# Optimization experiments

Hardware: AMD Instinct MI355X
Metric: run time of the kernel (lower is better)

The kernel has to match this reference:

```python
import jax, jax.numpy as jnp
import numpy as np

V, E, H, D = 32000, 512, 512, 3          # vocab, embed_dim, hidden_dim, max_depth
PD = max(H // 4, 16)                      # policy depth-embed dim = 128
DEPTH_EMBED_SCALE = 0.01
SIB_SCALE = 1.0 / np.sqrt(H)              # sibling_scale default 1/sqrt(hidden_dim)
GREEDY_THRESHOLD = 0.5
PROB_MIN, PROB_MAX = 1e-7, 1.0 - 1e-7


def _ln(x, g, b, eps=1e-5):
    m = x.mean(-1, keepdims=True)
    v = jnp.var(x, axis=-1, keepdims=True)
    return (x - m) * jax.lax.rsqrt(v + eps) * g + b


def setup_inputs() -> dict:
    key = jax.random.key(0)
    ks = jax.random.split(key, 12)
    def n(k, shape, s=0.02):
        return jax.random.normal(k, shape, jnp.float32) * s
    return {
        "token_ids": jax.random.randint(ks[0], (4096,), 0, V),
        "emb": n(ks[1], (V, E)),                      # embedding table
        "proj_w": n(ks[2], (H, E), 0.04), "proj_b": jnp.zeros(H, jnp.float32),
        "cf_w": n(ks[3], (2 * H, H), 0.04), "cf_b": jnp.zeros(2 * H, jnp.float32),
        "in_g": jnp.ones(H, jnp.float32), "in_b": jnp.zeros(H, jnp.float32),   # policy input LayerNorm
        "pde": n(ks[4], (D + 1, PD), 0.01),           # policy depth embedding
        "f1w": n(ks[5], (H // 2, H + PD), 0.04), "f1b": jnp.zeros(H // 2, jnp.float32),
        "n1g": jnp.ones(H // 2, jnp.float32), "n1b": jnp.zeros(H // 2, jnp.float32),
        "f2w": n(ks[6], (H // 4, H // 2), 0.06), "f2b": jnp.zeros(H // 4, jnp.float32),
        "n2g": jnp.ones(H // 4, jnp.float32), "n2b": jnp.zeros(H // 4, jnp.float32),
        "pow_w": n(ks[7], (1, H // 4), 0.01), "pow_b": jnp.zeros(1, jnp.float32),
        "sib": n(ks[8], (2, H)),                      # sibling embeddings (left/right)
        "dep": n(ks[9], (D + 1, H), 0.01),            # tree depth embeddings
        "out_w": n(ks[10], (V, H), 0.04), "out_b": jnp.zeros(V, jnp.float32),
    }


def _forward(token_ids, emb, proj_w, proj_b, cf_w, cf_b, in_g, in_b, pde,
             f1w, f1b, n1g, n1b, f2w, f2b, n2g, n2b, pow_w, pow_b,
             sib, dep, out_w, out_b):
    # h0: project token embeddings to hidden space. [N, H]
    h0 = emb[token_ids] @ proj_w.T + proj_b
    nodes = h0[None]                      # level-0 nodes: [1, N, H]
    agg_sum = h0                          # running sum over all tree nodes
    agg_cnt = jnp.float32(1.0)
    alive = jnp.float32(1.0)              # cumulative greedy-expand mask
    for level in range(D):
        # growth policy on the level-mean hidden (+ scaled depth embedding)
        lh = nodes.mean(0) + DEPTH_EMBED_SCALE * dep[level]          # [N, H]
        hn = _ln(lh, in_g, in_b)
        de = jnp.broadcast_to(pde[min(level, D)], (hn.shape[0], PD))
        x = jnp.concatenate([hn, de], axis=-1)
        x = jax.nn.relu(_ln(x @ f1w.T + f1b, n1g, n1b))
        x = jax.nn.relu(_ln(x @ f2w.T + f2b, n2g, n2b))
        p = jax.nn.sigmoid((x @ pow_w.T + pow_b)[..., 0])             # [N]
        p_mean = jnp.clip(p, PROB_MIN, PROB_MAX).mean()
        alive = alive * (p_mean >= GREEDY_THRESHOLD).astype(jnp.float32)
        # binary child expansion: child_fc then chunk into left/right + sibling embeds
        cf = jnp.einsum('mnh,kh->mnk', nodes, cf_w) + cf_b            # [M, N, 2H]
        left = cf[..., :H] + SIB_SCALE * sib[0]
        right = cf[..., H:] + SIB_SCALE * sib[1]
        nodes = jnp.concatenate([left, right], axis=0)                # [2M, N, H]
        agg_sum = agg_sum + alive * nodes.sum(0)
        agg_cnt = agg_cnt + alive * jnp.float32(nodes.shape[0])
    pooled = agg_sum / jnp.maximum(agg_cnt, 1e-8)                     # mean pooling
    return pooled @ out_w.T + out_b                                   # [N, V]


def reference(token_ids, emb, proj_w, proj_b, cf_w, cf_b, in_g, in_b, pde,
              f1w, f1b, n1g, n1b, f2w, f2b, n2g, n2b, pow_w, pow_b,
              sib, dep, out_w, out_b):
    return _forward(token_ids, emb, proj_w, proj_b, cf_w, cf_b, in_g, in_b, pde,
                    f1w, f1b, n1g, n1b, f2w, f2b, n2g, n2b, pow_w, pow_b,
                    sib, dep, out_w, out_b)
```

## Files before the change

### kernel.cpp

```cpp
#include <hip/hip_runtime.h>

typedef unsigned short u16;
using bf16x8 = __attribute__((ext_vector_type(8))) short;
using f32x4  = __attribute__((ext_vector_type(4))) float;

#define SIB_SCALE_F 0.04419417382415922f

__device__ __forceinline__ u16 f2b(float f) {
  unsigned u = __builtin_bit_cast(unsigned, f);
  return (u16)((u + 0x7FFFu + ((u >> 16) & 1u)) >> 16);
}

__device__ __forceinline__ float wred(float v) {
  #pragma unroll
  for (int m = 1; m < 64; m <<= 1) v += __shfl_xor(v, m);
  return v;
}

__device__ __forceinline__ void gload16(const void* g, void* l) {
  __builtin_amdgcn_global_load_lds(
      (const __attribute__((address_space(1))) unsigned int*)g,
      (__attribute__((address_space(3))) unsigned int*)l, 16, 0, 0);
}

__global__ __launch_bounds__(512, 2) void gemmP(
    const u16* __restrict__ A, const u16* __restrict__ B,
    const float* __restrict__ bias,
    float* __restrict__ C, int M, int N, int K, int MT)
{
  __shared__ u16 lds[65536];
  const int t = threadIdx.x, w = t >> 6, lane = t & 63;
  const int wm = w >> 2, wn = w & 3;
  const int r16 = lane & 15, ks = lane >> 4;

  const int bn = blockIdx.y * 256;
  const int mg = blockIdx.x;
  const int NT = K >> 6;

  auto stageH = [&](const u16* __restrict__ G, int grow0, int kt, int half, int opBase) {
    const int k0 = kt << 6;
    u16* dst = lds + opBase + ((kt & 1) << 14) + (half << 13);
    #pragma unroll
    for (int j = 0; j < 2; ++j) {
      const int r = half * 128 + j * 64 + w * 8 + (lane >> 3);
      const int s = (lane & 7) ^ (r & 7);
      gload16(G + (size_t)(grow0 + r) * K + k0 + s * 8,
              dst + j * 4096 + w * 512);
    }
  };

  for (int mt = 0; mt < MT; ++mt) {
    const int bm = (mg * MT + mt) * 256;

    f32x4 acc[8][4];
    #pragma unroll
    for (int m = 0; m < 8; ++m)
      #pragma unroll
      for (int n = 0; n < 4; ++n) {
        f32x4 z = {0.f, 0.f, 0.f, 0.f};
        acc[m][n] = z;
      }

    __builtin_amdgcn_sched_barrier(0);
    stageH(A, bm, 0, 0, 0);
    stageH(A, bm, 0, 1, 0);
    stageH(B, bn, 0, 0, 32768);
    stageH(B, bn, 0, 1, 32768);
    __builtin_amdgcn_sched_barrier(0);
    stageH(B, bn, 1, 0, 32768);
    stageH(B, bn, 1, 1, 32768);
    asm volatile("s_waitcnt vmcnt(4)" ::: "memory");
    __builtin_amdgcn_sched_barrier(0);
    __builtin_amdgcn_s_barrier();

    for (int kt = 0; kt < NT; ++kt) {
      const u16* Ab = lds + ((kt & 1) << 14);
      const u16* Bb = lds + 32768 + ((kt & 1) << 14);
      bf16x8 bfr[4][2];

      #pragma unroll
      for (int p = 0; p < 4; ++p) {
        bf16x8 af2[2][2];
        #pragma unroll
        for (int i = 0; i < 2; ++i) {
          const int row = wm * 128 + (2 * p + i) * 16 + r16;
          af2[i][0] = *(const bf16x8*)(Ab + row * 64 + ((ks ^ (row & 7)) << 3));
          af2[i][1] = *(const bf16x8*)(Ab + row * 64 + (((4 + ks) ^ (row & 7)) << 3));
        }
        if (p == 0) {
          #pragma unroll
          for (int n = 0; n < 4; ++n) {
            const int row = wn * 64 + n * 16 + r16;
            bfr[n][0] = *(const bf16x8*)(Bb + row * 64 + ((ks ^ (row & 7)) << 3));
            bfr[n][1] = *(const bf16x8*)(Bb + row * 64 + (((4 + ks) ^ (row & 7)) << 3));
          }
        }
        if (p == 0 && kt + 1 < NT) stageH(A, bm, kt + 1, 0, 0);
        if (p == 1 && kt + 1 < NT) stageH(A, bm, kt + 1, 1, 0);
        if (p == 2 && kt + 2 < NT) stageH(B, bn, kt + 2, 0, 32768);
        if (p == 3) {
          if (kt + 2 < NT) {
            stageH(B, bn, kt + 2, 1, 32768);
            asm volatile("s_waitcnt vmcnt(4)" ::: "memory");
          } else {
            asm volatile("s_waitcnt vmcnt(0)" ::: "memory");
          }
          __builtin_amdgcn_sched_barrier(0);
        }
        __builtin_amdgcn_s_barrier();
        asm volatile("s_waitcnt lgkmcnt(0)" ::: "memory");
        __builtin_amdgcn_sched_barrier(0);
        __builtin_amdgcn_s_setprio(1);
        #pragma unroll
        for (int i = 0; i < 2; ++i)
          #pragma unroll
          for (int n = 0; n < 4; ++n) {
            acc[2 * p + i][n] = __builtin_amdgcn_mfma_f32_16x16x32_bf16(
                bfr[n][0], af2[i][0], acc[2 * p + i][n], 0, 0, 0);
            acc[2 * p + i][n] = __builtin_amdgcn_mfma_f32_16x16x32_bf16(
                bfr[n][1], af2[i][1], acc[2 * p + i][n], 0, 0, 0);
          }
        __builtin_amdgcn_s_setprio(0);
        __builtin_amdgcn_s_barrier();
      }
    }

    #pragma unroll
    for (int m = 0; m < 8; ++m) {
      const int grow = bm + wm * 128 + m * 16 + r16;
      float* Crow = C + (size_t)grow * N;
      #pragma unroll
      for (int n = 0; n < 4; ++n) {
        const int gcol = bn + wn * 64 + n * 16 + ks * 4;
        const float4 bv = *(const float4*)(bias + gcol);
        float4 o;
        o.x = acc[m][n][0] + bv.x;
        o.y = acc[m][n][1] + bv.y;
        o.z = acc[m][n][2] + bv.z;
        o.w = acc[m][n][3] + bv.w;
        *(float4*)(Crow + gcol) = o;
      }
    }
  }
}

template <bool GATHER>
__global__ __launch_bounds__(256) void gemm_bf16_bt(
    const float* __restrict__ Afp, const int* __restrict__ tok,
    const u16* __restrict__ A, const u16* __restrict__ B,
    const float* __restrict__ bias, int blvl, float bscale,
    float* __restrict__ C, u16* __restrict__ Cb,
    int M, int N, int K)
{
  __shared__ u16 ldsA[128 * 32];
  __shared__ u16 ldsB[128 * 32];
  const int t = threadIdx.x;
  const int w = t >> 6;
  const int lane = t & 63;
  const int wr = w >> 1, wc = w & 1;

  const int nb = gridDim.x * gridDim.y;
  const int lid = blockIdx.y * gridDim.x + blockIdx.x;
  const int chunk = nb >> 3;
  const int nlid = (lid & 7) * chunk + (lid >> 3);
  const int bx = nlid % gridDim.x, by = nlid / gridDim.x;

  const int bm = bx * 128, bn = by * 128;
  const int r16 = lane & 15, ks = lane >> 4;
  const int srow = t >> 2, sslot = t & 3;

  f32x4 acc[4][4];
  #pragma unroll
  for (int m = 0; m < 4; ++m)
    #pragma unroll
    for (int n = 0; n < 4; ++n) {
      f32x4 z = {0.f, 0.f, 0.f, 0.f};
      acc[m][n] = z;
    }

  for (int k0 = 0; k0 < K; k0 += 32) {
    if (k0) __syncthreads();
    #pragma unroll
    for (int i = 0; i < 2; ++i) {
      const int row = srow + i * 64;
      const int sl = sslot ^ ((row >> 1) & 3);
      if constexpr (GATHER) {
        const float* src = Afp + (size_t)tok[bm + row] * 512 + k0 + sl * 8;
        const float4 a0 = *(const float4*)src;
        const float4 a1 = *(const float4*)(src + 4);
        bf16x8 v;
        v[0] = (short)f2b(a0.x); v[1] = (short)f2b(a0.y);
        v[2] = (short)f2b(a0.z); v[3] = (short)f2b(a0.w);
        v[4] = (short)f2b(a1.x); v[5] = (short)f2b(a1.y);
        v[6] = (short)f2b(a1.z); v[7] = (short)f2b(a1.w);
        *(bf16x8*)(ldsA + i * 2048 + w * 512 + lane * 8) = v;
      } else {
        gload16(A + (size_t)(bm + row) * K + k0 + sl * 8,
                ldsA + (i * 2048 + w * 512));
      }
      gload16(B + (size_t)(bn + row) * K + k0 + sl * 8,
              ldsB + (i * 2048 + w * 512));
    }
    __syncthreads();

    bf16x8 af[4], bfr[4];
    #pragma unroll
    for (int m = 0; m < 4; ++m) {
      const int row = wr * 64 + m * 16 + r16;
      af[m] = *(const bf16x8*)(ldsA + row * 32 + ((ks ^ ((row >> 1) & 3)) << 3));
    }
    #pragma unroll
    for (int n = 0; n < 4; ++n) {
      const int row = wc * 64 + n * 16 + r16;
      bfr[n] = *(const bf16x8*)(ldsB + row * 32 + ((ks ^ ((row >> 1) & 3)) << 3));
    }
    #pragma unroll
    for (int m = 0; m < 4; ++m)
      #pragma unroll
      for (int n = 0; n < 4; ++n)
        acc[m][n] = __builtin_amdgcn_mfma_f32_16x16x32_bf16(bfr[n], af[m], acc[m][n], 0, 0, 0);
  }

  const float* be = bias + (size_t)(bm >> 12) * blvl;
  #pragma unroll
  for (int m = 0; m < 4; ++m) {
    const int grow = bm + wr * 64 + m * 16 + r16;
    #pragma unroll
    for (int n = 0; n < 4; ++n) {
      const int gcol = bn + wc * 64 + n * 16 + ks * 4;
      const float4 bv = *(const float4*)(be + gcol);
      float4 o;
      o.x = acc[m][n][0] + bv.x * bscale;
      o.y = acc[m][n][1] + bv.y * bscale;
      o.z = acc[m][n][2] + bv.z * bscale;
      o.w = acc[m][n][3] + bv.w * bscale;
      const size_t idx = (size_t)grow * N + gcol;
      *(float4*)(C + idx) = o;
      if (Cb) {
        ushort4 ob = { f2b(o.x), f2b(o.y), f2b(o.z), f2b(o.w) };
        *(ushort4*)(Cb + idx) = ob;
      }
    }
  }
}

__global__ __launch_bounds__(256) void prep_misc(
    const float* __restrict__ cf_w, const float* __restrict__ cf_b,
    const float* __restrict__ sib, const float* __restrict__ proj_w,
    const float* __restrict__ f1w, const float* __restrict__ f1b,
    const float* __restrict__ f2w, const float* __restrict__ pde,
    u16* __restrict__ wsum_b, u16* __restrict__ projw_b,
    u16* __restrict__ f1w512b, u16* __restrict__ f2wb,
    float* __restrict__ cvec, float* __restrict__ psum,
    float* __restrict__ y1bias)
{
  const int b = blockIdx.x, t = threadIdx.x;
  if (b < 256) {
    const int idx = b * 256 + t;
    const float4 a = ((const float4*)cf_w)[idx];
    const float4 c = ((const float4*)(cf_w + 262144))[idx];
    ushort4 o = { f2b(a.x + c.x), f2b(a.y + c.y), f2b(a.z + c.z), f2b(a.w + c.w) };
    ((ushort4*)wsum_b)[idx] = o;
  } else if (b < 512) {
    const int idx = (b - 256) * 256 + t;
    const float4 v = ((const float4*)proj_w)[idx];
    ushort4 o = { f2b(v.x), f2b(v.y), f2b(v.z), f2b(v.w) };
    ((ushort4*)projw_b)[idx] = o;
  } else if (b < 640) {
    const int fi = (b - 512) * 256 + t;
    const int row = fi >> 7, c4 = fi & 127;
    const float4 v = *(const float4*)(f1w + (size_t)row * 640 + c4 * 4);
    ushort4 o = { f2b(v.x), f2b(v.y), f2b(v.z), f2b(v.w) };
    ((ushort4*)f1w512b)[row * 128 + c4] = o;
  } else if (b < 672) {
    const int idx = (b - 640) * 256 + t;
    const float4 v = ((const float4*)f2w)[idx];
    ushort4 o = { f2b(v.x), f2b(v.y), f2b(v.z), f2b(v.w) };
    ((ushort4*)f2wb)[idx] = o;
  } else if (b < 675) {
    const int l = b - 672, j = t;
    const float* wrow = f1w + (size_t)j * 640 + 512;
    const float* p = pde + l * 128;
    float s = f1b[j];
    #pragma unroll 4
    for (int k = 0; k < 128; ++k) s += wrow[k] * p[k];
    y1bias[l * 256 + j] = s;
  } else {
    cvec[t]       = cf_b[t]       + cf_b[512 + t] + SIB_SCALE_F * (sib[t]       + sib[512 + t]);
    cvec[256 + t] = cf_b[256 + t] + cf_b[768 + t] + SIB_SCALE_F * (sib[256 + t] + sib[768 + t]);
    if (t < 3) psum[t] = 0.f;
  }
}

__global__ __launch_bounds__(256) void mean_ln_concat_b(
    const float* __restrict__ S0, const float* __restrict__ S1,
    const float* __restrict__ S2,
    const float* __restrict__ dep,
    const float* __restrict__ g, const float* __restrict__ b,
    u16* __restrict__ X)
{
  const int wid = threadIdx.x >> 6, lane = threadIdx.x & 63;
  const int gr = blockIdx.x * 4 + wid;
  const int l = gr >> 12, n = gr & 4095;
  const float* Sr = (l == 0 ? S0 : l == 1 ? S1 : S2) + (size_t)n * 512;
  const float invM = (l == 0 ? 1.f : l == 1 ? 0.5f : 0.25f);
  const float* depl = dep + 512 * l;
  const int c0 = lane * 8;
  float x[8];
  float s = 0.f, sq = 0.f;
  #pragma unroll
  for (int i = 0; i < 8; ++i) {
    const float v = Sr[c0 + i] * invM + 0.01f * depl[c0 + i];
    x[i] = v; s += v; sq += v * v;
  }
  s = wred(s); sq = wred(sq);
  const float mean = s * (1.f / 512.f);
  const float var = sq * (1.f / 512.f) - mean * mean;
  const float rs = rsqrtf(var + 1e-5f);
  ushort4 o0, o1;
  o0.x = f2b((x[0] - mean) * rs * g[c0 + 0] + b[c0 + 0]);
  o0.y = f2b((x[1] - mean) * rs * g[c0 + 1] + b[c0 + 1]);
  o0.z = f2b((x[2] - mean) * rs * g[c0 + 2] + b[c0 + 2]);
  o0.w = f2b((x[3] - mean) * rs * g[c0 + 3] + b[c0 + 3]);
  o1.x = f2b((x[4] - mean) * rs * g[c0 + 4] + b[c0 + 4]);
  o1.y = f2b((x[5] - mean) * rs * g[c0 + 5] + b[c0 + 5]);
  o1.z = f2b((x[6] - mean) * rs * g[c0 + 6] + b[c0 + 6]);
  o1.w = f2b((x[7] - mean) * rs * g[c0 + 7] + b[c0 + 7]);
  ushort4* Xr = (ushort4*)(X + (size_t)gr * 512);
  Xr[lane * 2]     = o0;
  Xr[lane * 2 + 1] = o1;
}

__global__ __launch_bounds__(256) void ln_relu_b256(
    const float* __restrict__ X, const float* __restrict__ g,
    const float* __restrict__ b, u16* __restrict__ O)
{
  const int wid = threadIdx.x >> 6, lane = threadIdx.x & 63;
  const int n = blockIdx.x * 4 + wid;
  const float* Xr = X + (size_t)n * 256;
  float x[4];
  float s = 0.f, sq = 0.f;
  #pragma unroll
  for (int i = 0; i < 4; ++i) {
    x[i] = Xr[lane * 4 + i]; s += x[i]; sq += x[i] * x[i];
  }
  s = wred(s); sq = wred(sq);
  const float mean = s * (1.f / 256.f);
  const float var = sq * (1.f / 256.f) - mean * mean;
  const float rs = rsqrtf(var + 1e-5f);
  ushort4 o;
  o.x = f2b(fmaxf((x[0] - mean) * rs * g[lane * 4 + 0] + b[lane * 4 + 0], 0.f));
  o.y = f2b(fmaxf((x[1] - mean) * rs * g[lane * 4 + 1] + b[lane * 4 + 1], 0.f));
  o.z = f2b(fmaxf((x[2] - mean) * rs * g[lane * 4 + 2] + b[lane * 4 + 2], 0.f));
  o.w = f2b(fmaxf((x[3] - mean) * rs * g[lane * 4 + 3] + b[lane * 4 + 3], 0.f));
  ((ushort4*)(O + (size_t)n * 256))[lane] = o;
}

__global__ __launch_bounds__(256) void ln_relu128(
    float* __restrict__ X, const float* __restrict__ g, const float* __restrict__ b)
{
  const int wid = threadIdx.x >> 6, lane = threadIdx.x & 63;
  const int n = blockIdx.x * 4 + wid;
  float* Xr = X + (size_t)n * 128;
  float x[2];
  float s = 0.f, sq = 0.f;
  #pragma unroll
  for (int i = 0; i < 2; ++i) {
    x[i] = Xr[lane * 2 + i]; s += x[i]; sq += x[i] * x[i];
  }
  s = wred(s); sq = wred(sq);
  const float mean = s * (1.f / 128.f);
  const float var = sq * (1.f / 128.f) - mean * mean;
  const float rs = rsqrtf(var + 1e-5f);
  #pragma unroll
  for (int i = 0; i < 2; ++i) {
    const int c = lane * 2 + i;
    Xr[c] = fmaxf((x[i] - mean) * rs * g[c] + b[c], 0.f);
  }
}

__global__ __launch_bounds__(256) void policy_reduce_b(
    const float* __restrict__ Y2, const float* __restrict__ pw,
    const float* __restrict__ pb, float* __restrict__ psum)
{
  __shared__ float part[4];
  const int wid = threadIdx.x >> 6, lane = threadIdx.x & 63;
  const int gr = blockIdx.x * 4 + wid;
  const float* r = Y2 + (size_t)gr * 128;
  float z = r[lane * 2] * pw[lane * 2] + r[lane * 2 + 1] * pw[lane * 2 + 1];
  z = wred(z);
  if (lane == 0) {
    const float p = 1.f / (1.f + expf(-(z + pb[0])));
    part[wid] = fminf(fmaxf(p, 1e-7f), 1.f - 1e-7f);
  }
  __syncthreads();
  if (threadIdx.x == 0)
    atomicAdd(psum + (gr >> 12), part[0] + part[1] + part[2] + part[3]);
}

__global__ void finalize_coef(const float* __restrict__ psum, float* __restrict__ coef)
{
  float alive = 1.f, cnt = 1.f;
  #pragma unroll
  for (int l = 0; l < 3; ++l) {
    const float pm = psum[l] * (1.f / 4096.f);
    if (!(pm >= 0.5f)) alive = 0.f;
    coef[l] = alive;
    cnt += alive * (float)(2 << l);
  }
  coef[3] = 1.f / fmaxf(cnt, 1e-8f);
}

__global__ __launch_bounds__(256) void pool_to_bf16(
    const float* __restrict__ h0, const float* __restrict__ S1,
    const float* __restrict__ S2, const float* __restrict__ S3,
    const float* __restrict__ coef, u16* __restrict__ P)
{
  const int idx = blockIdx.x * 256 + threadIdx.x;
  const float c0 = coef[0], c1 = coef[1], c2 = coef[2], inv = coef[3];
  const float4 a  = ((const float4*)h0)[idx];
  const float4 s1 = ((const float4*)S1)[idx];
  const float4 s2 = ((const float4*)S2)[idx];
  const float4 s3 = ((const float4*)S3)[idx];
  ushort4 o;
  o.x = f2b((a.x + c0 * s1.x + c1 * s2.x + c2 * s3.x) * inv);
  o.y = f2b((a.y + c0 * s1.y + c1 * s2.y + c2 * s3.y) * inv);
  o.z = f2b((a.z + c0 * s1.z + c1 * s2.z + c2 * s3.z) * inv);
  o.w = f2b((a.w + c0 * s1.w + c1 * s2.w + c2 * s3.w) * inv);
  ((ushort4*)P)[idx] = o;
}

__global__ __launch_bounds__(256) void f32_to_bf16_vec(
    const float* __restrict__ src, u16* __restrict__ dst, int n4)
{
  const int idx = blockIdx.x * 256 + threadIdx.x;
  if (idx >= n4) return;
  const float4 v = ((const float4*)src)[idx];
  ushort4 o = { f2b(v.x), f2b(v.y), f2b(v.z), f2b(v.w) };
  ((ushort4*)dst)[idx] = o;
}

extern "C" void kernel_launch(void* const* d_in, const int* in_sizes, int n_in,
                              void* d_out, int out_size, void* d_ws, size_t ws_size,
                              hipStream_t stream) {
  const int*   tok    = (const int*)  d_in[0];
  const float* emb    = (const float*)d_in[1];
  const float* proj_w = (const float*)d_in[2];
  const float* proj_b = (const float*)d_in[3];
  const float* cf_w   = (const float*)d_in[4];
  const float* cf_b   = (const float*)d_in[5];
  const float* in_g   = (const float*)d_in[6];
  const float* in_b   = (const float*)d_in[7];
  const float* pde    = (const float*)d_in[8];
  const float* f1w    = (const float*)d_in[9];
  const float* f1b    = (const float*)d_in[10];
  const float* n1g    = (const float*)d_in[11];
  const float* n1b    = (const float*)d_in[12];
  const float* f2w    = (const float*)d_in[13];
  const float* f2bias = (const float*)d_in[14];
  const float* n2g    = (const float*)d_in[15];
  const float* n2b    = (const float*)d_in[16];
  const float* pow_w  = (const float*)d_in[17];
  const float* pow_b  = (const float*)d_in[18];
  const float* sib    = (const float*)d_in[19];
  const float* dep    = (const float*)d_in[20];
  const float* out_w  = (const float*)d_in[21];
  const float* out_b  = (const float*)d_in[22];
  float* out = (float*)d_out;

  char* ws = (char*)d_ws;
  size_t off = 0;
  auto alloc = [&](size_t bytes) -> void* {
    void* p = ws + off;
    off += (bytes + 255) & ~(size_t)255;
    return p;
  };
  u16*   outw_b  = (u16*)  alloc((size_t)32000 * 512 * 2);
  u16*   projw_b = (u16*)  alloc((size_t)512 * 512 * 2);
  u16*   wsum_b  = (u16*)  alloc((size_t)512 * 512 * 2);
  u16*   f1w512b = (u16*)  alloc((size_t)256 * 512 * 2);
  u16*   f2wb    = (u16*)  alloc((size_t)128 * 256 * 2);
  float* h0f     = (float*)alloc((size_t)4096 * 512 * 4);
  u16*   h0b     = (u16*)  alloc((size_t)4096 * 512 * 2);
  float* S1f     = (float*)alloc((size_t)4096 * 512 * 4);
  u16*   S1b     = (u16*)  alloc((size_t)4096 * 512 * 2);
  float* S2f     = (float*)alloc((size_t)4096 * 512 * 4);
  u16*   S2b     = (u16*)  alloc((size_t)4096 * 512 * 2);
  float* S3f     = (float*)alloc((size_t)4096 * 512 * 4);
  u16*   S3b     = (u16*)  alloc((size_t)4096 * 512 * 2);
  u16*   X       = (u16*)  alloc((size_t)12288 * 512 * 2);
  float* Y1      = (float*)alloc((size_t)12288 * 256 * 4);
  u16*   Y1b     = (u16*)  alloc((size_t)12288 * 256 * 2);
  float* Y2      = (float*)alloc((size_t)12288 * 128 * 4);
  float* y1bias  = (float*)alloc(3 * 256 * 4);
  float* cvec    = (float*)alloc(512 * 4);
  float* psum    = (float*)alloc(256);
  float* coef    = (float*)alloc(256);
  u16*   poolb   = (u16*)  alloc((size_t)4096 * 512 * 2);

  prep_misc<<<676, 256, 0, stream>>>(cf_w, cf_b, sib, proj_w, f1w, f1b, f2w, pde,
                                     wsum_b, projw_b, f1w512b, f2wb,
                                     cvec, psum, y1bias);
  f32_to_bf16_vec<<<16000, 256, 0, stream>>>(out_w, outw_b, 4096000);

  gemm_bf16_bt<true><<<dim3(32, 4), 256, 0, stream>>>(
      emb, tok, nullptr, projw_b, proj_b, 0, 1.f, h0f, h0b, 4096, 512, 512);
  gemm_bf16_bt<false><<<dim3(32, 4), 256, 0, stream>>>(
      nullptr, nullptr, h0b, wsum_b, cvec, 0, 1.f, S1f, S1b, 4096, 512, 512);
  gemm_bf16_bt<false><<<dim3(32, 4), 256, 0, stream>>>(
      nullptr, nullptr, S1b, wsum_b, cvec, 0, 2.f, S2f, S2b, 4096, 512, 512);
  gemm_bf16_bt<false><<<dim3(32, 4), 256, 0, stream>>>(
      nullptr, nullptr, S2b, wsum_b, cvec, 0, 4.f, S3f, S3b, 4096, 512, 512);

  mean_ln_concat_b<<<3072, 256, 0, stream>>>(h0f, S1f, S2f, dep, in_g, in_b, X);
  gemm_bf16_bt<false><<<dim3(96, 2), 256, 0, stream>>>(
      nullptr, nullptr, X, f1w512b, y1bias, 256, 1.f, Y1, nullptr, 12288, 256, 512);
  ln_relu_b256<<<3072, 256, 0, stream>>>(Y1, n1g, n1b, Y1b);
  gemm_bf16_bt<false><<<dim3(96, 1), 256, 0, stream>>>(
      nullptr, nullptr, Y1b, f2wb, f2bias, 0, 1.f, Y2, nullptr, 12288, 128, 256);
  ln_relu128<<<3072, 256, 0, stream>>>(Y2, n2g, n2b);
  policy_reduce_b<<<3072, 256, 0, stream>>>(Y2, pow_w, pow_b, psum);
  finalize_coef<<<1, 1, 0, stream>>>(psum, coef);

  pool_to_bf16<<<2048, 256, 0, stream>>>(h0f, S1f, S2f, S3f, coef, poolb);

  gemmP<<<dim3(2, 125), 512, 0, stream>>>(poolb, outw_b, out_b,
                                          out, 4096, 32000, 512, 8);
}
```

Measured before the change: 424.4 us.

## Fuse pooling into level-3 GEMM epilogue and merge policy LN, reduce, and conversion kernels

Moves the level-3 child GEMM after the policy network and gives it an epilogue that computes the alive flags from psum and writes the pooled bf16 output directly. This removes the S3 fp32/bf16 buffers and the separate finalize_coef and pool_to_bf16 kernels. It also fuses ln_relu128 with policy_reduce into one kernel, avoiding the Y2 write-back and re-read. The out_w bf16 conversion is folded into prep_misc as extra blocks. Together these cut kernel launches and memory traffic, at the cost of a heavier GEMM epilogue that reads three fp32 tensors.

```diff
diff --git a/kernel.cpp b/kernel.cpp
--- a/kernel.cpp
+++ b/kernel.cpp
@@ -144,12 +144,15 @@
   }
 }
 
-template <bool GATHER>
+template <bool GATHER, bool POOL>
 __global__ __launch_bounds__(256) void gemm_bf16_bt(
     const float* __restrict__ Afp, const int* __restrict__ tok,
     const u16* __restrict__ A, const u16* __restrict__ B,
     const float* __restrict__ bias, int blvl, float bscale,
     float* __restrict__ C, u16* __restrict__ Cb,
+    const float* __restrict__ h0f, const float* __restrict__ S1f,
+    const float* __restrict__ S2f, const float* __restrict__ psum,
+    u16* __restrict__ P,
     int M, int N, int K)
 {
   __shared__ u16 ldsA[128 * 32];
@@ -222,6 +225,16 @@
   }
 
   const float* be = bias + (size_t)(bm >> 12) * blvl;
+
+  float a0 = 0.f, a1 = 0.f, a2 = 0.f, inv = 0.f;
+  if constexpr (POOL) {
+    a0 = (psum[0] * (1.f / 4096.f) >= 0.5f) ? 1.f : 0.f;
+    a1 = a0 * ((psum[1] * (1.f / 4096.f) >= 0.5f) ? 1.f : 0.f);
+    a2 = a1 * ((psum[2] * (1.f / 4096.f) >= 0.5f) ? 1.f : 0.f);
+    const float cnt = 1.f + a0 * 2.f + a1 * 4.f + a2 * 8.f;
+    inv = 1.f / fmaxf(cnt, 1e-8f);
+  }
+
   #pragma unroll
   for (int m = 0; m < 4; ++m) {
     const int grow = bm + wr * 64 + m * 16 + r16;
@@ -235,10 +248,22 @@
       o.z = acc[m][n][2] + bv.z * bscale;
       o.w = acc[m][n][3] + bv.w * bscale;
       const size_t idx = (size_t)grow * N + gcol;
-      *(float4*)(C + idx) = o;
-      if (Cb) {
-        ushort4 ob = { f2b(o.x), f2b(o.y), f2b(o.z), f2b(o.w) };
-        *(ushort4*)(Cb + idx) = ob;
+      if constexpr (POOL) {
+        const float4 h = *(const float4*)(h0f + idx);
+        const float4 s1 = *(const float4*)(S1f + idx);
+        const float4 s2 = *(const float4*)(S2f + idx);
+        ushort4 ob;
+        ob.x = f2b((h.x + a0 * s1.x + a1 * s2.x + a2 * o.x) * inv);
+        ob.y = f2b((h.y + a0 * s1.y + a1 * s2.y + a2 * o.y) * inv);
+        ob.z = f2b((h.z + a0 * s1.z + a1 * s2.z + a2 * o.z) * inv);
+        ob.w = f2b((h.w + a0 * s1.w + a1 * s2.w + a2 * o.w) * inv);
+        *(ushort4*)(P + idx) = ob;
+      } else {
+        *(float4*)(C + idx) = o;
+        if (Cb) {
+          ushort4 ob = { f2b(o.x), f2b(o.y), f2b(o.z), f2b(o.w) };
+          *(ushort4*)(Cb + idx) = ob;
+        }
       }
     }
   }
@@ -249,13 +274,19 @@
     const float* __restrict__ sib, const float* __restrict__ proj_w,
     const float* __restrict__ f1w, const float* __restrict__ f1b,
     const float* __restrict__ f2w, const float* __restrict__ pde,
+    const float* __restrict__ out_w,
     u16* __restrict__ wsum_b, u16* __restrict__ projw_b,
     u16* __restrict__ f1w512b, u16* __restrict__ f2wb,
     float* __restrict__ cvec, float* __restrict__ psum,
-    float* __restrict__ y1bias)
+    float* __restrict__ y1bias, u16* __restrict__ outw_b)
 {
   const int b = blockIdx.x, t = threadIdx.x;
-  if (b < 256) {
+  if (b >= 676) {
+    const int idx = (b - 676) * 256 + t;
+    const float4 v = ((const float4*)out_w)[idx];
+    ushort4 o = { f2b(v.x), f2b(v.y), f2b(v.z), f2b(v.w) };
+    ((ushort4*)outw_b)[idx] = o;
+  } else if (b < 256) {
     const int idx = b * 256 + t;
     const float4 a = ((const float4*)cf_w)[idx];
     const float4 c = ((const float4*)(cf_w + 262144))[idx];
@@ -356,38 +387,32 @@
   ((ushort4*)(O + (size_t)n * 256))[lane] = o;
 }
 
-__global__ __launch_bounds__(256) void ln_relu128(
-    float* __restrict__ X, const float* __restrict__ g, const float* __restrict__ b)
-{
-  const int wid = threadIdx.x >> 6, lane = threadIdx.x & 63;
-  const int n = blockIdx.x * 4 + wid;
-  float* Xr = X + (size_t)n * 128;
-  float x[2];
-  float s = 0.f, sq = 0.f;
-  #pragma unroll
-  for (int i = 0; i < 2; ++i) {
-    x[i] = Xr[lane * 2 + i]; s += x[i]; sq += x[i] * x[i];
-  }
-  s = wred(s); sq = wred(sq);
-  const float mean = s * (1.f / 128.f);
-  const float var = sq * (1.f / 128.f) - mean * mean;
-  const float rs = rsqrtf(var + 1e-5f);
-  #pragma unroll
-  for (int i = 0; i < 2; ++i) {
-    const int c = lane * 2 + i;
-    Xr[c] = fmaxf((x[i] - mean) * rs * g[c] + b[c], 0.f);
-  }
-}
-
-__global__ __launch_bounds__(256) void policy_reduce_b(
-    const float* __restrict__ Y2, const float* __restrict__ pw,
+__global__ __launch_bounds__(256) void ln_policy128(
+    const float* __restrict__ Y2, const float* __restrict__ g,
+    const float* __restrict__ b, const float* __restrict__ pw,
     const float* __restrict__ pb, float* __restrict__ psum)
 {
   __shared__ float part[4];
   const int wid = threadIdx.x >> 6, lane = threadIdx.x & 63;
   const int gr = blockIdx.x * 4 + wid;
-  const float* r = Y2 + (size_t)gr * 128;
-  float z = r[lane * 2] * pw[lane * 2] + r[lane * 2 + 1] * pw[lane * 2 + 1];
+  const float* Xr = Y2 + (size_t)gr * 128;
+  float x[2];
+  float s = 0.f, sq = 0.f;
+  #pragma unroll
+  for (int i = 0; i < 2; ++i) {
+    x[i] = Xr[lane * 2 + i]; s += x[i]; sq += x[i] * x[i];
+  }
+  s = wred(s); sq = wred(sq);
+  const float mean = s * (1.f / 128.f);
+  const float var = sq * (1.f / 128.f) - mean * mean;
+  const float rs = rsqrtf(var + 1e-5f);
+  float z = 0.f;
+  #pragma unroll
+  for (int i = 0; i < 2; ++i) {
+    const int c = lane * 2 + i;
+    const float v = fmaxf((x[i] - mean) * rs * g[c] + b[c], 0.f);
+    z += v * pw[c];
+  }
   z = wred(z);
   if (lane == 0) {
     const float p = 1.f / (1.f + expf(-(z + pb[0])));
@@ -396,48 +421,6 @@
   __syncthreads();
   if (threadIdx.x == 0)
     atomicAdd(psum + (gr >> 12), part[0] + part[1] + part[2] + part[3]);
-}
-
-__global__ void finalize_coef(const float* __restrict__ psum, float* __restrict__ coef)
-{
-  float alive = 1.f, cnt = 1.f;
-  #pragma unroll
-  for (int l = 0; l < 3; ++l) {
-    const float pm = psum[l] * (1.f / 4096.f);
-    if (!(pm >= 0.5f)) alive = 0.f;
-    coef[l] = alive;
-    cnt += alive * (float)(2 << l);
-  }
-  coef[3] = 1.f / fmaxf(cnt, 1e-8f);
-}
-
-__global__ __launch_bounds__(256) void pool_to_bf16(
-    const float* __restrict__ h0, const float* __restrict__ S1,
-    const float* __restrict__ S2, const float* __restrict__ S3,
-    const float* __restrict__ coef, u16* __restrict__ P)
-{
-  const int idx = blockIdx.x * 256 + threadIdx.x;
-  const float c0 = coef[0], c1 = coef[1], c2 = coef[2], inv = coef[3];
-  const float4 a  = ((const float4*)h0)[idx];
-  const float4 s1 = ((const float4*)S1)[idx];
-  const float4 s2 = ((const float4*)S2)[idx];
-  const float4 s3 = ((const float4*)S3)[idx];
-  ushort4 o;
-  o.x = f2b((a.x + c0 * s1.x + c1 * s2.x + c2 * s3.x) * inv);
-  o.y = f2b((a.y + c0 * s1.y + c1 * s2.y + c2 * s3.y) * inv);
-  o.z = f2b((a.z + c0 * s1.z + c1 * s2.z + c2 * s3.z) * inv);
-  o.w = f2b((a.w + c0 * s1.w + c1 * s2.w + c2 * s3.w) * inv);
-  ((ushort4*)P)[idx] = o;
-}
-
-__global__ __launch_bounds__(256) void f32_to_bf16_vec(
-    const float* __restrict__ src, u16* __restrict__ dst, int n4)
-{
-  const int idx = blockIdx.x * 256 + threadIdx.x;
-  if (idx >= n4) return;
-  const float4 v = ((const float4*)src)[idx];
-  ushort4 o = { f2b(v.x), f2b(v.y), f2b(v.z), f2b(v.w) };
-  ((ushort4*)dst)[idx] = o;
 }
 
 extern "C" void kernel_launch(void* const* d_in, const int* in_sizes, int n_in,
@@ -486,8 +469,6 @@
   u16*   S1b     = (u16*)  alloc((size_t)4096 * 512 * 2);
   float* S2f     = (float*)alloc((size_t)4096 * 512 * 4);
   u16*   S2b     = (u16*)  alloc((size_t)4096 * 512 * 2);
-  float* S3f     = (float*)alloc((size_t)4096 * 512 * 4);
-  u16*   S3b     = (u16*)  alloc((size_t)4096 * 512 * 2);
   u16*   X       = (u16*)  alloc((size_t)12288 * 512 * 2);
   float* Y1      = (float*)alloc((size_t)12288 * 256 * 4);
   u16*   Y1b     = (u16*)  alloc((size_t)12288 * 256 * 2);
@@ -495,34 +476,36 @@
   float* y1bias  = (float*)alloc(3 * 256 * 4);
   float* cvec    = (float*)alloc(512 * 4);
   float* psum    = (float*)alloc(256);
-  float* coef    = (float*)alloc(256);
   u16*   poolb   = (u16*)  alloc((size_t)4096 * 512 * 2);
 
-  prep_misc<<<676, 256, 0, stream>>>(cf_w, cf_b, sib, proj_w, f1w, f1b, f2w, pde,
-                                     wsum_b, projw_b, f1w512b, f2wb,
-                                     cvec, psum, y1bias);
-  f32_to_bf16_vec<<<16000, 256, 0, stream>>>(out_w, outw_b, 4096000);
-
-  gemm_bf16_bt<true><<<dim3(32, 4), 256, 0, stream>>>(
-      emb, tok, nullptr, projw_b, proj_b, 0, 1.f, h0f, h0b, 4096, 512, 512);
-  gemm_bf16_bt<false><<<dim3(32, 4), 256, 0, stream>>>(
-      nullptr, nullptr, h0b, wsum_b, cvec, 0, 1.f, S1f, S1b, 4096, 512, 512);
-  gemm_bf16_bt<false><<<dim3(32, 4), 256, 0, stream>>>(
-      nullptr, nullptr, S1b, wsum_b, cvec, 0, 2.f, S2f, S2b, 4096, 512, 512);
-  gemm_bf16_bt<false><<<dim3(32, 4), 256, 0, stream>>>(
-      nullptr, nullptr, S2b, wsum_b, cvec, 0, 4.f, S3f, S3b, 4096, 512, 512);
+  prep_misc<<<16676, 256, 0, stream>>>(cf_w, cf_b, sib, proj_w, f1w, f1b, f2w,
+                                       pde, out_w,
+                                       wsum_b, projw_b, f1w512b, f2wb,
+                                       cvec, psum, y1bias, outw_b);
+
+  gemm_bf16_bt<true, false><<<dim3(32, 4), 256, 0, stream>>>(
+      emb, tok, nullptr, projw_b, proj_b, 0, 1.f, h0f, h0b,
+      nullptr, nullptr, nullptr, nullptr, nullptr, 4096, 512, 512);
+  gemm_bf16_bt<false, false><<<dim3(32, 4), 256, 0, stream>>>(
+      nullptr, nullptr, h0b, wsum_b, cvec, 0, 1.f, S1f, S1b,
+      nullptr, nullptr, nullptr, nullptr, nullptr, 4096, 512, 512);
+  gemm_bf16_bt<false, false><<<dim3(32, 4), 256, 0, stream>>>(
+      nullptr, nullptr, S1b, wsum_b, cvec, 0, 2.f, S2f, S2b,
+      nullptr, nullptr, nullptr, nullptr, nullptr, 4096, 512, 512);
 
   mean_ln_concat_b<<<3072, 256, 0, stream>>>(h0f, S1f, S2f, dep, in_g, in_b, X);
-  gemm_bf16_bt<false><<<dim3(96, 2), 256, 0, stream>>>(
-      nullptr, nullptr, X, f1w512b, y1bias, 256, 1.f, Y1, nullptr, 12288, 256, 512);
+  gemm_bf16_bt<false, false><<<dim3(96, 2), 256, 0, stream>>>(
+      nullptr, nullptr, X, f1w512b, y1bias, 256, 1.f, Y1, nullptr,
+      nullptr, nullptr, nullptr, nullptr, nullptr, 12288, 256, 512);
   ln_relu_b256<<<3072, 256, 0, stream>>>(Y1, n1g, n1b, Y1b);
-  gemm_bf16_bt<false><<<dim3(96, 1), 256, 0, stream>>>(
-      nullptr, nullptr, Y1b, f2wb, f2bias, 0, 1.f, Y2, nullptr, 12288, 128, 256);
-  ln_relu128<<<3072, 256, 0, stream>>>(Y2, n2g, n2b);
-  policy_reduce_b<<<3072, 256, 0, stream>>>(Y2, pow_w, pow_b, psum);
-  finalize_coef<<<1, 1, 0, stream>>>(psum, coef);
-
-  pool_to_bf16<<<2048, 256, 0, stream>>>(h0f, S1f, S2f, S3f, coef, poolb);
+  gemm_bf16_bt<false, false><<<dim3(96, 1), 256, 0, stream>>>(
+      nullptr, nullptr, Y1b, f2wb, f2bias, 0, 1.f, Y2, nullptr,
+      nullptr, nullptr, nullptr, nullptr, nullptr, 12288, 128, 256);
+  ln_policy128<<<3072, 256, 0, stream>>>(Y2, n2g, n2b, pow_w, pow_b, psum);
+
+  gemm_bf16_bt<false, true><<<dim3(32, 4), 256, 0, stream>>>(
+      nullptr, nullptr, S2b, wsum_b, cvec, 0, 4.f, nullptr, nullptr,
+      h0f, S1f, S2f, psum, poolb, 4096, 512, 512);
 
   gemmP<<<dim3(2, 125), 512, 0, stream>>>(poolb, outw_b, out_b,
                                           out, 4096, 32000, 512, 8);
```

After: 409.9 us. -3.4%, faster.
